# Kernel tuning notes

Hardware: AMD Instinct MI355X
Metric: run time of the kernel (lower is better)

The kernel has to match this reference:

```python
import jax, jax.numpy as jnp
import numpy as np

B, E, R, D, L = 256, 15000, 237, 200, 64


def setup_inputs() -> dict:
    key = jax.random.key(0)
    ks = jax.random.split(key, 8)
    emb_e = jax.random.normal(ks[0], (E, D), jnp.float32) * 0.1
    emb_rel = jax.random.normal(ks[1], (R, D), jnp.float32) * 0.1
    nf_weights = jax.random.normal(ks[2], (R, L), jnp.float32) * 0.1
    lit = jax.random.uniform(ks[3], (E, L), jnp.float32)          # numerical literals (buffer, non-learned)
    c = jax.random.normal(ks[4], (L,), jnp.float32) * 0.5         # fixed RBF centers
    var = jax.random.uniform(ks[5], (L,), jnp.float32) + 0.5      # fixed RBF variances (>0)
    e1 = jax.random.randint(ks[6], (B,), 0, E)
    rel = jax.random.randint(ks[7], (B,), 0, R)
    return {"emb_e": emb_e, "emb_rel": emb_rel, "nf_weights": nf_weights,
            "lit": lit, "c": c, "var": var, "e1": e1, "rel": rel}


def reference(emb_e, emb_rel, nf_weights, lit, c, var, e1, rel):
    # structural score: (e1_emb * rel_emb) @ emb_e^T -> (B, E)
    e1_emb = emb_e[e1]                                   # (B, D)
    rel_emb = emb_rel[rel]                               # (B, D)
    score_l = jnp.einsum('bd,ed->be', e1_emb * rel_emb, emb_e)
    # numerical-literal score: RBF kernel on literal differences, weighted by rel
    n = lit[e1][:, None, :] - lit[None, :, :]            # (B, E, L)
    phi = jnp.exp(-(n - c) ** 2 / var)                   # (B, E, L)
    score_n = jnp.einsum('bel,bl->be', phi, nf_weights[rel])
    return jax.nn.sigmoid(score_l + score_n)
```

## Files before the change

kernel.cpp:

```cpp
#include <hip/hip_runtime.h>

#define E_ 15000
#define D_ 200
#define L_ 64
#define B_ 256
#define LOG2E 1.4426950408889634f

typedef float v2f __attribute__((ext_vector_type(2)));

#define QTC_OFF 0
#define SUC_OFF 204800
#define WTC_OFF 270336
#define R_OFF   335872

__global__ __launch_bounds__(256) void setup_k(
    const float* __restrict__ emb_e, const float* __restrict__ emb_rel,
    const float* __restrict__ nfw,   const float* __restrict__ lit,
    const float* __restrict__ c,     const float* __restrict__ var,
    const int* __restrict__ e1,      const int* __restrict__ rel,
    float* __restrict__ qtc, float* __restrict__ suc,
    float* __restrict__ wtc, float* __restrict__ r)
{
    const int b = blockIdx.x;
    const int t = threadIdx.x;
    const int ie = e1[b];
    const int ir = rel[b];
    const int cb = (b >> 4);
    const int bb = (b & 15);
    if (t < D_) qtc[cb * 3200 + t * 16 + bb] =
        emb_e[ie * D_ + t] * emb_rel[ir * D_ + t];
    if (t < L_) {
        const float rl = sqrtf(LOG2E / var[t]);
        suc[cb * 1024 + t * 16 + bb] = (lit[ie * L_ + t] - c[t]) * rl;
        wtc[cb * 1024 + t * 16 + bb] = nfw[ir * L_ + t];
        if (b == 0) r[t] = rl;
    }
}

__global__ __launch_bounds__(256) void main_k(
    const float* __restrict__ emb_e, const float* __restrict__ lit,
    const float* __restrict__ qtc,   const float* __restrict__ suc,
    const float* __restrict__ wtc,   const float* __restrict__ r,
    float* __restrict__ out)
{
    __shared__ float qt_s[3200];
    __shared__ float su_s[1024];
    __shared__ float wt_s[1024];
    __shared__ float r_s[64];

    const int w    = blockIdx.x;
    const int orig = (w & 7) * 118 + (w >> 3);
    const int x = orig >> 4;
    const int y = orig & 15;

    const int tid = threadIdx.x;
    const int e   = x * 256 + tid;
    const int ec  = (e < E_) ? e : (E_ - 1);
    const int b0  = y * 16;

    {
        const float4* qsrc = (const float4*)qtc + y * 800;
        float4* qdst = (float4*)qt_s;
        #pragma unroll
        for (int i = 0; i < 3; ++i) qdst[tid + 256 * i] = qsrc[tid + 256 * i];
        if (tid < 32) qdst[768 + tid] = qsrc[768 + tid];
        ((float4*)su_s)[tid] = ((const float4*)suc)[y * 256 + tid];
        ((float4*)wt_s)[tid] = ((const float4*)wtc)[y * 256 + tid];
        if (tid < 16) ((float4*)r_s)[tid] = ((const float4*)r)[tid];
    }
    __syncthreads();

    v2f acc[8];
    #pragma unroll
    for (int j = 0; j < 8; ++j) acc[j] = (v2f)(0.0f);

    const float* ep = emb_e + (size_t)ec * D_;
    #pragma unroll 2
    for (int d = 0; d < D_; d += 4) {
        const float4 v4 = *(const float4*)(ep + d);
        const float va[4] = {v4.x, v4.y, v4.z, v4.w};
        #pragma unroll
        for (int k = 0; k < 4; ++k) {
            const v2f* q2 = (const v2f*)(qt_s + (d + k) * 16);
            const v2f ev = {va[k], va[k]};
            #pragma unroll
            for (int j = 0; j < 8; ++j)
                acc[j] = __builtin_elementwise_fma(ev, q2[j], acc[j]);
        }
    }

    const float* lp = lit + (size_t)ec * L_;
    #pragma unroll 2
    for (int l = 0; l < L_; l += 4) {
        const float4 x4 = *(const float4*)(lp + l);
        const float xa[4] = {x4.x, x4.y, x4.z, x4.w};
        #pragma unroll
        for (int k = 0; k < 4; ++k) {
            const float u = xa[k] * r_s[l + k];
            const v2f uv = {u, u};
            const v2f* s2 = (const v2f*)(su_s + (l + k) * 16);
            const v2f* w2 = (const v2f*)(wt_s + (l + k) * 16);
            #pragma unroll
            for (int j = 0; j < 8; ++j) {
                const v2f t = s2[j] - uv;
                const v2f m = -(t * t);
                const v2f ph = {__builtin_amdgcn_exp2f(m.x),
                                __builtin_amdgcn_exp2f(m.y)};
                acc[j] = __builtin_elementwise_fma(ph, w2[j], acc[j]);
            }
        }
    }

    if (e < E_) {
        #pragma unroll
        for (int j = 0; j < 8; ++j) {
            #pragma unroll
            for (int h = 0; h < 2; ++h) {
                const float z = h ? acc[j].y : acc[j].x;
                const float ezn = __builtin_amdgcn_exp2f(-z * LOG2E);
                out[(size_t)(b0 + 2 * j + h) * E_ + e] =
                    __builtin_amdgcn_rcpf(1.0f + ezn);
            }
        }
    }
}

extern "C" void kernel_launch(void* const* d_in, const int* in_sizes, int n_in,
                              void* d_out, int out_size, void* d_ws, size_t ws_size,
                              hipStream_t stream) {
    const float* emb_e   = (const float*)d_in[0];
    const float* emb_rel = (const float*)d_in[1];
    const float* nfw     = (const float*)d_in[2];
    const float* lit     = (const float*)d_in[3];
    const float* c       = (const float*)d_in[4];
    const float* var     = (const float*)d_in[5];
    const int*   e1      = (const int*)d_in[6];
    const int*   rel     = (const int*)d_in[7];
    float* out = (float*)d_out;

    char* ws = (char*)d_ws;
    float* qtc = (float*)(ws + QTC_OFF);
    float* suc = (float*)(ws + SUC_OFF);
    float* wtc = (float*)(ws + WTC_OFF);
    float* r   = (float*)(ws + R_OFF);

    setup_k<<<dim3(B_), dim3(256), 0, stream>>>(emb_e, emb_rel, nfw, lit, c, var,
                                                e1, rel, qtc, suc, wtc, r);

    main_k<<<dim3(944), dim3(256), 0, stream>>>(emb_e, lit, qtc, suc, wtc, r, out);
}
```

Measured before the change: 71.13 us.

## Factor RBF exponent algebraically and use inline packed FMA with vector LDS loads

```diff
diff --git a/kernel.cpp b/kernel.cpp
--- a/kernel.cpp
+++ b/kernel.cpp
@@ -7,6 +7,21 @@
 #define LOG2E 1.4426950408889634f
 
 typedef float v2f __attribute__((ext_vector_type(2)));
+typedef float v4f __attribute__((ext_vector_type(4)));
+
+#define LO2(q) __builtin_shufflevector(q, q, 0, 1)
+#define HI2(q) __builtin_shufflevector(q, q, 2, 3)
+
+__device__ __forceinline__ void pk_fma(v2f& acc, v2f a, v2f b) {
+    asm("v_pk_fma_f32 %0, %1, %2, %0"
+        : "+v"(acc) : "v"(a), "v"(b));
+}
+__device__ __forceinline__ v2f pk_fma3(v2f a, v2f b, v2f c) {
+    v2f d;
+    asm("v_pk_fma_f32 %0, %1, %2, %3"
+        : "=v"(d) : "v"(a), "v"(b), "v"(c));
+    return d;
+}
 
 #define QTC_OFF 0
 #define SUC_OFF 204800
@@ -31,8 +46,9 @@
         emb_e[ie * D_ + t] * emb_rel[ir * D_ + t];
     if (t < L_) {
         const float rl = sqrtf(LOG2E / var[t]);
-        suc[cb * 1024 + t * 16 + bb] = (lit[ie * L_ + t] - c[t]) * rl;
-        wtc[cb * 1024 + t * 16 + bb] = nfw[ir * L_ + t];
+        const float su = (lit[ie * L_ + t] - c[t]) * rl;
+        suc[cb * 1024 + t * 16 + bb] = 2.0f * su;
+        wtc[cb * 1024 + t * 16 + bb] = nfw[ir * L_ + t] * exp2f(-su * su);
         if (b == 0) r[t] = rl;
     }
 }
@@ -70,9 +86,9 @@
     }
     __syncthreads();
 
-    v2f acc[8];
+    v2f acc2[8];
     #pragma unroll
-    for (int j = 0; j < 8; ++j) acc[j] = (v2f)(0.0f);
+    for (int j = 0; j < 8; ++j) acc2[j] = (v2f)(0.0f);
 
     const float* ep = emb_e + (size_t)ec * D_;
     #pragma unroll 2
@@ -81,11 +97,14 @@
         const float va[4] = {v4.x, v4.y, v4.z, v4.w};
         #pragma unroll
         for (int k = 0; k < 4; ++k) {
-            const v2f* q2 = (const v2f*)(qt_s + (d + k) * 16);
             const v2f ev = {va[k], va[k]};
+            const v4f* qrow = (const v4f*)(qt_s + (d + k) * 16);
             #pragma unroll
-            for (int j = 0; j < 8; ++j)
-                acc[j] = __builtin_elementwise_fma(ev, q2[j], acc[j]);
+            for (int g = 0; g < 4; ++g) {
+                const v4f q = qrow[g];
+                pk_fma(acc2[2 * g],     LO2(q), ev);
+                pk_fma(acc2[2 * g + 1], HI2(q), ev);
+            }
         }
     }
 
@@ -96,17 +115,25 @@
         const float xa[4] = {x4.x, x4.y, x4.z, x4.w};
         #pragma unroll
         for (int k = 0; k < 4; ++k) {
-            const float u = xa[k] * r_s[l + k];
-            const v2f uv = {u, u};
-            const v2f* s2 = (const v2f*)(su_s + (l + k) * 16);
-            const v2f* w2 = (const v2f*)(wt_s + (l + k) * 16);
+            const float u   = xa[k] * r_s[l + k];
+            const float u2n = -u * u;
+            const v2f uv   = {u, u};
+            const v2f u2nv = {u2n, u2n};
+            const v4f* srow = (const v4f*)(su_s + (l + k) * 16);
+            const v4f* wrow = (const v4f*)(wt_s + (l + k) * 16);
             #pragma unroll
-            for (int j = 0; j < 8; ++j) {
-                const v2f t = s2[j] - uv;
-                const v2f m = -(t * t);
-                const v2f ph = {__builtin_amdgcn_exp2f(m.x),
-                                __builtin_amdgcn_exp2f(m.y)};
-                acc[j] = __builtin_elementwise_fma(ph, w2[j], acc[j]);
+            for (int g = 0; g < 4; ++g) {
+                const v4f s4 = srow[g];
+                const v4f w4 = wrow[g];
+                const v2f a0 = pk_fma3(LO2(s4), uv, u2nv);
+                const v2f a1 = pk_fma3(HI2(s4), uv, u2nv);
+                v2f ph0, ph1;
+                ph0.x = __builtin_amdgcn_exp2f(a0.x);
+                ph0.y = __builtin_amdgcn_exp2f(a0.y);
+                ph1.x = __builtin_amdgcn_exp2f(a1.x);
+                ph1.y = __builtin_amdgcn_exp2f(a1.y);
+                pk_fma(acc2[2 * g],     ph0, LO2(w4));
+                pk_fma(acc2[2 * g + 1], ph1, HI2(w4));
             }
         }
     }
@@ -116,7 +143,7 @@
         for (int j = 0; j < 8; ++j) {
             #pragma unroll
             for (int h = 0; h < 2; ++h) {
-                const float z = h ? acc[j].y : acc[j].x;
+                const float z = h ? acc2[j].y : acc2[j].x;
                 const float ezn = __builtin_amdgcn_exp2f(-z * LOG2E);
                 out[(size_t)(b0 + 2 * j + h) * E_ + e] =
                     __builtin_amdgcn_rcpf(1.0f + ezn);
```

New measurement: 72.26 us. About the same (+1.6%).

## Expand RBF square algebraically and split reduction across two block halves

Applied to the files above, without the earlier changes.

```diff
diff --git a/kernel.cpp b/kernel.cpp
--- a/kernel.cpp
+++ b/kernel.cpp
@@ -5,8 +5,6 @@
 #define L_ 64
 #define B_ 256
 #define LOG2E 1.4426950408889634f
-
-typedef float v2f __attribute__((ext_vector_type(2)));
 
 #define QTC_OFF 0
 #define SUC_OFF 204800
@@ -31,13 +29,14 @@
         emb_e[ie * D_ + t] * emb_rel[ir * D_ + t];
     if (t < L_) {
         const float rl = sqrtf(LOG2E / var[t]);
-        suc[cb * 1024 + t * 16 + bb] = (lit[ie * L_ + t] - c[t]) * rl;
-        wtc[cb * 1024 + t * 16 + bb] = nfw[ir * L_ + t];
+        const float su = (lit[ie * L_ + t] - c[t]) * rl;
+        suc[cb * 1024 + t * 16 + bb] = 2.0f * su;
+        wtc[cb * 1024 + t * 16 + bb] = nfw[ir * L_ + t] * exp2f(-su * su);
         if (b == 0) r[t] = rl;
     }
 }
 
-__global__ __launch_bounds__(256) void main_k(
+__global__ __launch_bounds__(512) void main_k(
     const float* __restrict__ emb_e, const float* __restrict__ lit,
     const float* __restrict__ qtc,   const float* __restrict__ suc,
     const float* __restrict__ wtc,   const float* __restrict__ r,
@@ -47,80 +46,82 @@
     __shared__ float su_s[1024];
     __shared__ float wt_s[1024];
     __shared__ float r_s[64];
+    __shared__ float comb[16][256];
 
     const int w    = blockIdx.x;
     const int orig = (w & 7) * 118 + (w >> 3);
     const int x = orig >> 4;
     const int y = orig & 15;
 
-    const int tid = threadIdx.x;
-    const int e   = x * 256 + tid;
-    const int ec  = (e < E_) ? e : (E_ - 1);
-    const int b0  = y * 16;
+    const int tid  = threadIdx.x;
+    const int el   = tid & 255;
+    const int half = tid >> 8;
+    const int e    = x * 256 + el;
+    const int ec   = (e < E_) ? e : (E_ - 1);
+    const int b0   = y * 16;
 
     {
         const float4* qsrc = (const float4*)qtc + y * 800;
         float4* qdst = (float4*)qt_s;
-        #pragma unroll
-        for (int i = 0; i < 3; ++i) qdst[tid + 256 * i] = qsrc[tid + 256 * i];
-        if (tid < 32) qdst[768 + tid] = qsrc[768 + tid];
-        ((float4*)su_s)[tid] = ((const float4*)suc)[y * 256 + tid];
-        ((float4*)wt_s)[tid] = ((const float4*)wtc)[y * 256 + tid];
+        qdst[tid] = qsrc[tid];
+        if (tid < 288) qdst[512 + tid] = qsrc[512 + tid];
+        if (tid < 256) ((float4*)su_s)[tid] = ((const float4*)suc)[y * 256 + tid];
+        else ((float4*)wt_s)[tid - 256] = ((const float4*)wtc)[y * 256 + tid - 256];
         if (tid < 16) ((float4*)r_s)[tid] = ((const float4*)r)[tid];
     }
     __syncthreads();
 
-    v2f acc[8];
+    float acc[16];
     #pragma unroll
-    for (int j = 0; j < 8; ++j) acc[j] = (v2f)(0.0f);
+    for (int j = 0; j < 16; ++j) acc[j] = 0.0f;
 
-    const float* ep = emb_e + (size_t)ec * D_;
+    const float* ep = emb_e + (size_t)ec * D_ + 100 * half;
     #pragma unroll 2
-    for (int d = 0; d < D_; d += 4) {
-        const float4 v4 = *(const float4*)(ep + d);
+    for (int d4 = 0; d4 < 100; d4 += 4) {
+        const float4 v4 = *(const float4*)(ep + d4);
         const float va[4] = {v4.x, v4.y, v4.z, v4.w};
         #pragma unroll
         for (int k = 0; k < 4; ++k) {
-            const v2f* q2 = (const v2f*)(qt_s + (d + k) * 16);
-            const v2f ev = {va[k], va[k]};
+            const float* qrow = qt_s + (100 * half + d4 + k) * 16;
             #pragma unroll
-            for (int j = 0; j < 8; ++j)
-                acc[j] = __builtin_elementwise_fma(ev, q2[j], acc[j]);
+            for (int bb = 0; bb < 16; ++bb)
+                acc[bb] = fmaf(va[k], qrow[bb], acc[bb]);
         }
     }
 
-    const float* lp = lit + (size_t)ec * L_;
+    const float* lp = lit + (size_t)ec * L_ + 32 * half;
     #pragma unroll 2
-    for (int l = 0; l < L_; l += 4) {
-        const float4 x4 = *(const float4*)(lp + l);
+    for (int l4 = 0; l4 < 32; l4 += 4) {
+        const float4 x4 = *(const float4*)(lp + l4);
         const float xa[4] = {x4.x, x4.y, x4.z, x4.w};
         #pragma unroll
         for (int k = 0; k < 4; ++k) {
-            const float u = xa[k] * r_s[l + k];
-            const v2f uv = {u, u};
-            const v2f* s2 = (const v2f*)(su_s + (l + k) * 16);
-            const v2f* w2 = (const v2f*)(wt_s + (l + k) * 16);
+            const int   la  = 32 * half + l4 + k;
+            const float u   = xa[k] * r_s[la];
+            const float u2n = -u * u;
+            const float* srow = su_s + la * 16;
+            const float* wrow = wt_s + la * 16;
             #pragma unroll
-            for (int j = 0; j < 8; ++j) {
-                const v2f t = s2[j] - uv;
-                const v2f m = -(t * t);
-                const v2f ph = {__builtin_amdgcn_exp2f(m.x),
-                                __builtin_amdgcn_exp2f(m.y)};
-                acc[j] = __builtin_elementwise_fma(ph, w2[j], acc[j]);
+            for (int bb = 0; bb < 16; ++bb) {
+                const float a  = fmaf(srow[bb], u, u2n);
+                const float ph = __builtin_amdgcn_exp2f(a);
+                acc[bb] = fmaf(ph, wrow[bb], acc[bb]);
             }
         }
     }
 
-    if (e < E_) {
+    if (half) {
         #pragma unroll
-        for (int j = 0; j < 8; ++j) {
-            #pragma unroll
-            for (int h = 0; h < 2; ++h) {
-                const float z = h ? acc[j].y : acc[j].x;
-                const float ezn = __builtin_amdgcn_exp2f(-z * LOG2E);
-                out[(size_t)(b0 + 2 * j + h) * E_ + e] =
-                    __builtin_amdgcn_rcpf(1.0f + ezn);
-            }
+        for (int bb = 0; bb < 16; ++bb) comb[bb][el] = acc[bb];
+    }
+    __syncthreads();
+
+    if (!half && e < E_) {
+        #pragma unroll
+        for (int bb = 0; bb < 16; ++bb) {
+            const float z   = acc[bb] + comb[bb][el];
+            const float ezn = __builtin_amdgcn_exp2f(-z * LOG2E);
+            out[(size_t)(b0 + bb) * E_ + e] = __builtin_amdgcn_rcpf(1.0f + ezn);
         }
     }
 }
@@ -147,5 +148,5 @@
     setup_k<<<dim3(B_), dim3(256), 0, stream>>>(emb_e, emb_rel, nfw, lit, c, var,
                                                 e1, rel, qtc, suc, wtc, r);
 
-    main_k<<<dim3(944), dim3(256), 0, stream>>>(emb_e, lit, qtc, suc, wtc, r, out);
+    main_k<<<dim3(944), dim3(512), 0, stream>>>(emb_e, lit, qtc, suc, wtc, r, out);
 }
```

After: 96.98 us. 1.36x slower.
